# Optimization experiments

Measured on AMD Instinct MI355X. Metric: run time of the kernel, lower is better.

## Reference

```python
import jax, jax.numpy as jnp
from jax import lax
import numpy as np

B, T, H, OUT = 8, 1500, 1280, 4096
MAXTOK = 375
N_INNER = 3  # 1 mandatory integrate-and-fire iteration + 2 gated extras (alpha<1 => 1 suffices)


def _forward_cif(hidden, alphas, num_tokens, max_tok):
    # hidden: [B, T, D], alphas: [B, T], num_tokens: [B] int32
    Bv, Tv, _ = hidden.shape
    nm1 = num_tokens - 1
    bidx = jnp.arange(Bv)

    def step(carry, xs):
        integrate, token_index = carry  # [B] float, [B] int32
        alpha_t, not_last = xs
        col = jnp.zeros((Bv, max_tok), alphas.dtype)
        alpha = alpha_t
        alpha_needed = 1.0 - integrate
        integrate = integrate + alpha
        ready = integrate >= 1.0
        remainds = jnp.zeros_like(alpha)
        active = jnp.any(ready) | True  # first body iteration always runs (do-while)
        active = jnp.asarray(True)
        for _ in range(N_INNER):
            n_int = jnp.where(ready, integrate - 1.0, integrate)
            a_int = jnp.where(ready, alpha_needed, alpha)
            n_col = col.at[bidx, token_index].set(a_int)
            n_rem = alpha - a_int
            n_tok = jnp.minimum(token_index + ready.astype(token_index.dtype), nm1)
            n_ready = n_int >= 1.0
            integrate = jnp.where(active, n_int, integrate)
            col = jnp.where(active, n_col, col)
            remainds = jnp.where(active, n_rem, remainds)
            token_index = jnp.where(active, n_tok, token_index)
            alpha = jnp.where(active, n_rem, alpha)
            alpha_needed = jnp.where(active, jnp.ones_like(alpha_needed), alpha_needed)
            ready = jnp.where(active, n_ready, jnp.zeros_like(ready))
            active = active & jnp.any(ready)
        # torch adds remainds into column t at step t+1 (so last column never gets it)
        col = jnp.where(not_last, col.at[bidx, token_index].add(remainds), col)
        return (integrate, token_index), col

    init = (jnp.zeros((Bv,), alphas.dtype), jnp.zeros((Bv,), jnp.int32))
    xs = (alphas.T, jnp.arange(Tv) < Tv - 1)  # per-step alpha column, not-last flag
    _, cols = lax.scan(step, init, xs)  # cols: [T, B, max_tok]
    weights = jnp.transpose(cols, (1, 2, 0))  # [B, max_tok, T]
    return jnp.einsum('bmt,btd->bmd', weights, hidden)


def setup_inputs() -> dict:
    key = jax.random.key(0)
    ks = jax.random.split(key, 4)
    audio_features = jax.random.normal(ks[0], (B, T, H), jnp.float32)
    num_tokens = jax.random.randint(ks[1], (B,), 100, MAXTOK + 1).astype(jnp.int32)
    rms_w = jnp.ones((H,), jnp.float32) * 0.4
    cif_w = jax.random.normal(ks[2], (H - 1, H), jnp.float32) / np.sqrt(H - 1)
    cif_b = jnp.zeros((H,), jnp.float32)
    text_w = jax.random.normal(ks[3], (H, OUT), jnp.float32) / np.sqrt(H)
    text_b = jnp.zeros((OUT,), jnp.float32)
    return dict(audio_features=audio_features, num_tokens=num_tokens, rms_w=rms_w,
                cif_w=cif_w, cif_b=cif_b, text_w=text_w, text_b=text_b, max_tokens=MAXTOK)


def reference(audio_features, num_tokens, rms_w, cif_w, cif_b, text_w, text_b, max_tokens):
    alphas = jax.nn.sigmoid(audio_features[:, :, -1])  # [B, T]
    pred_num_tokens = alphas.sum(-1)  # [B]
    alphas = alphas * (num_tokens.astype(alphas.dtype) / pred_num_tokens)[:, None]
    h = _forward_cif(audio_features[:, :, :-1], alphas, num_tokens, max_tokens)  # [B, M, H-1]
    h = h @ cif_w + cif_b  # cif_proj -> [B, M, H]
    d = h.shape[-1]
    rms = jnp.sqrt(jnp.sum(h * h, axis=-1, keepdims=True) / d + 1e-6)
    h = h / rms * rms_w  # RMSNorm(post_ln)
    h = h @ text_w + text_b  # text_proj -> [B, M, OUT]
    return h, pred_num_tokens
```

## Files before the change

### kernel.cpp

```cpp
#include <hip/hip_runtime.h>
#include <hip/hip_bf16.h>
#include <stdint.h>

#define B_ 8
#define T_ 1500
#define TPAD 1504
#define H_ 1280
#define HM1 1279
#define OUT_ 4096
#define MTOK 375
#define MROWS (B_*MTOK)
#define KPAD 1280

typedef __attribute__((ext_vector_type(8))) short bf16x8;
typedef __attribute__((ext_vector_type(4))) float f32x4;
typedef unsigned short u16;
typedef unsigned int u32;

static __device__ __forceinline__ u16 f2bf(float f) {
    unsigned int x = __float_as_uint(f);
    unsigned int r = (x + 0x7fffu + ((x >> 16) & 1u)) >> 16;
    return (u16)r;
}
static __device__ __forceinline__ void glds16(const u16* g, u16* l) {
    __builtin_amdgcn_global_load_lds(
        (const __attribute__((address_space(1))) void*)g,
        (__attribute__((address_space(3))) void*)l, 16, 0, 0);
}

__global__ __launch_bounds__(256) void k_front(
    const float* __restrict__ audio, const int* __restrict__ num_tokens,
    const float* __restrict__ rms_w,
    float* __restrict__ pred_out,
    int* __restrict__ tok0, float* __restrict__ w0a,
    int* __restrict__ tok1, float* __restrict__ w1a,
    int* __restrict__ lo, int* __restrict__ hi,
    float* __restrict__ h_sumsq,
    const float* __restrict__ cif_w, const float* __restrict__ text_w,
    u16* __restrict__ cwt, u16* __restrict__ twt)
{
    __shared__ float smem[3524];
    const int tid = threadIdx.x;

    if (blockIdx.x < B_) {
        const int b = blockIdx.x;
        float* al = smem;
        float* ip = smem + TPAD;
        float* red = smem + 2*TPAD;
        int*   redI = (int*)(smem + 2*TPAD + 256);
        float* scale_sh = smem + 2*TPAD + 512;

        float sig[6];
        float s = 0.f;
        #pragma unroll
        for (int i = 0; i < 6; ++i) {
            int t = tid + i*256;
            sig[i] = 0.f;
            if (t < T_) {
                float x = audio[((size_t)b*T_ + t)*H_ + (H_-1)];
                sig[i] = 1.f / (1.f + expf(-x));
                s += sig[i];
            }
        }
        red[tid] = s; __syncthreads();
        for (int off = 128; off > 0; off >>= 1) {
            if (tid < off) red[tid] += red[tid+off];
            __syncthreads();
        }
        if (tid == 0) {
            float pred = red[0];
            pred_out[b] = pred;
            *scale_sh = (float)num_tokens[b] / pred;
        }
        __syncthreads();
        float scale = *scale_sh;
        #pragma unroll
        for (int i = 0; i < 6; ++i) {
            int t = tid + i*256;
            if (t < T_) al[t] = sig[i] * scale;
        }
        if (tid < TPAD - T_) al[T_ + tid] = 0.f;
        for (int m = tid; m < MTOK; m += 256) {
            lo[b*MTOK+m] = T_; hi[b*MTOK+m] = 0;
            h_sumsq[b*MTOK+m] = 0.f;
        }
        if (tid == 0) lo[b*MTOK] = 0;
        __syncthreads();

        if (tid == 0) {
            float integ = 0.f;
            float4 c0 = *(const float4*)&al[0];
            float4 c1 = *(const float4*)&al[4];
            float4 c2 = *(const float4*)&al[8];
            float4 c3 = *(const float4*)&al[12];
            for (int t = 0; t < TPAD; t += 16) {
                float4 n0, n1, n2, n3;
                if (t + 16 < TPAD) {
                    n0 = *(const float4*)&al[t+16];
                    n1 = *(const float4*)&al[t+20];
                    n2 = *(const float4*)&al[t+24];
                    n3 = *(const float4*)&al[t+28];
                }
                float4 o0, o1, o2, o3;
                float sx;
                o0.x = integ; sx = integ + c0.x; integ = sx - floorf(sx);
                o0.y = integ; sx = integ + c0.y; integ = sx - floorf(sx);
                o0.z = integ; sx = integ + c0.z; integ = sx - floorf(sx);
                o0.w = integ; sx = integ + c0.w; integ = sx - floorf(sx);
                o1.x = integ; sx = integ + c1.x; integ = sx - floorf(sx);
                o1.y = integ; sx = integ + c1.y; integ = sx - floorf(sx);
                o1.z = integ; sx = integ + c1.z; integ = sx - floorf(sx);
                o1.w = integ; sx = integ + c1.w; integ = sx - floorf(sx);
                o2.x = integ; sx = integ + c2.x; integ = sx - floorf(sx);
                o2.y = integ; sx = integ + c2.y; integ = sx - floorf(sx);
                o2.z = integ; sx = integ + c2.z; integ = sx - floorf(sx);
                o2.w = integ; sx = integ + c2.w; integ = sx - floorf(sx);
                o3.x = integ; sx = integ + c3.x; integ = sx - floorf(sx);
                o3.y = integ; sx = integ + c3.y; integ = sx - floorf(sx);
                o3.z = integ; sx = integ + c3.z; integ = sx - floorf(sx);
                o3.w = integ; sx = integ + c3.w; integ = sx - floorf(sx);
                *(float4*)&ip[t+0]  = o0;
                *(float4*)&ip[t+4]  = o1;
                *(float4*)&ip[t+8]  = o2;
                *(float4*)&ip[t+12] = o3;
                c0 = n0; c1 = n1; c2 = n2; c3 = n3;
            }
        }
        __syncthreads();

        const int t0 = tid * 6;
        const int nm1 = num_tokens[b] - 1;
        int fires[6];
        int cnt = 0;
        if (t0 < T_) {
            #pragma unroll
            for (int j = 0; j < 6; ++j) {
                int t = t0 + j;
                float sx = ip[t] + al[t];
                fires[j] = (sx >= 1.f) ? 1 : 0;
                cnt += fires[j];
            }
        }
        redI[tid] = cnt; __syncthreads();
        #pragma unroll
        for (int off = 1; off < 256; off <<= 1) {
            int v = redI[tid];
            if (tid >= off) v += redI[tid - off];
            __syncthreads();
            redI[tid] = v;
            __syncthreads();
        }
        if (t0 < T_) {
            int F = redI[tid] - cnt;
            const int base = b*T_;
            #pragma unroll
            for (int j = 0; j < 6; ++j) {
                int t = t0 + j;
                float a = al[t], ipv = ip[t];
                int fire = fires[j];
                F += fire;
                int tk1 = min(F, nm1);
                int tk0 = min(F - fire, nm1);
                float w0 = fire ? (1.f - ipv) : a;
                float w1 = (t < T_-1) ? (a - w0) : 0.f;
                tok0[base+t] = tk0;  w0a[base+t] = w0;
                tok1[base+t] = tk1;  w1a[base+t] = w1;
                if (tk1 != tk0) {
                    hi[b*MTOK + tk0] = t + 1;
                    lo[b*MTOK + tk1] = t;
                }
                if (t == T_-1) hi[b*MTOK + tk1] = T_;
            }
        }
    } else {
        float (*tile)[33] = (float(*)[33])smem;
        int blk = blockIdx.x - B_;
        const float* src; u16* dst; int R, C, bx, by; bool scaled;
        if (blk < 1600) { src = cif_w;  dst = cwt; R = HM1; C = H_;   bx = blk % 40;  by = blk / 40;  scaled = false; }
        else { blk -= 1600; src = text_w; dst = twt; R = H_;  C = OUT_; bx = blk % 128; by = blk / 128; scaled = true; }
        int c0 = bx * 32, r0 = by * 32;
        int lx = tid & 31, ly = tid >> 5;
        #pragma unroll
        for (int j = 0; j < 4; ++j) {
            int r = r0 + ly + j*8;
            tile[ly + j*8][lx] = (r < R) ? src[(size_t)r*C + c0 + lx] : 0.f;
        }
        __syncthreads();
        float rw = scaled ? rms_w[r0 + lx] : 1.f;
        #pragma unroll
        for (int j = 0; j < 4; ++j) {
            int c = c0 + ly + j*8;
            dst[(size_t)c*KPAD + r0 + lx] = f2bf(tile[lx][ly + j*8] * rw);
        }
    }
}

__global__ __launch_bounds__(256) void k3_pool(
    const float* __restrict__ audio,
    const int* __restrict__ tok0, const float* __restrict__ w0a,
    const int* __restrict__ tok1, const float* __restrict__ w1a,
    const int* __restrict__ lo, const int* __restrict__ hi,
    u16* __restrict__ h1b)
{
    __shared__ float wl[1536];
    const int bm = blockIdx.x;
    const int b = bm / MTOK, m = bm % MTOK;
    const int l = lo[bm], h = hi[bm];
    const int tid = threadIdx.x;
    const int len = h - l;

    for (int j = tid; j < len; j += 256) {
        int i0 = b*T_ + l + j;
        float w = 0.f;
        if (tok0[i0] == m) w += w0a[i0];
        if (tok1[i0] == m) w += w1a[i0];
        wl[j] = w;
    }
    __syncthreads();

    const int d4 = tid * 4;
    const int d1 = 1024 + tid;
    const float* rowp = audio + (size_t)(b*T_ + l) * H_;
    float4 acc4 = make_float4(0.f, 0.f, 0.f, 0.f);
    float acc1 = 0.f;
    #pragma unroll 4
    for (int j = 0; j < len; ++j) {
        float w = wl[j];
        const float* row = rowp + (size_t)j * H_;
        float4 r4 = *(const float4*)(row + d4);
        float r1 = (d1 < HM1) ? row[d1] : 0.f;
        acc4.x += w * r4.x; acc4.y += w * r4.y;
        acc4.z += w * r4.z; acc4.w += w * r4.w;
        acc1 += w * r1;
    }
    u16* dst = h1b + (size_t)bm * KPAD;
    ushort4 o;
    o.x = f2bf(acc4.x); o.y = f2bf(acc4.y); o.z = f2bf(acc4.z); o.w = f2bf(acc4.w);
    *(ushort4*)&dst[d4] = o;
    dst[d1] = (d1 < HM1) ? f2bf(acc1) : (u16)0;
}

template<bool CIF>
__global__ __launch_bounds__(512, 2) void gemm256(
    const u16* __restrict__ A, const u16* __restrict__ Bt,
    const float* __restrict__ bias, void* __restrict__ Cv,
    float* __restrict__ h_sumsq, int M, int N)
{
    constexpr int K = KPAD;
    constexpr int NT = K / 64;
    __shared__ u16 sA[2][256*64];
    __shared__ u16 sB[2][256*64];
    const int tid = threadIdx.x;
    const int wave = tid >> 6, lane = tid & 63;
    const int wr = wave >> 2, wc = wave & 3;
    const int lrow = lane & 15, quad = lane >> 4;
    const int m0 = blockIdx.y * 256, n0 = blockIdx.x * 256;

    const int rS = tid >> 3;
    const int cS = (tid & 7) ^ (rS & 7);
    u32 aoff[4], boff[4];
    #pragma unroll
    for (int p = 0; p < 4; ++p) {
        aoff[p] = (u32)(min(m0 + rS + 64*p, M - 1) * K + cS*8);
        boff[p] = (u32)((n0 + rS + 64*p) * K + cS*8);
    }

    const int csw = (quad ^ (lrow & 7)) << 3;
    int offA[8], offB[4];
    #pragma unroll
    for (int mi = 0; mi < 8; ++mi)
        offA[mi] = (wr*128 + mi*16 + lrow)*64 + csw;
    #pragma unroll
    for (int ni = 0; ni < 4; ++ni)
        offB[ni] = (wc*64 + ni*16 + lrow)*64 + csw;

    f32x4 acc[8][4] = {};

    #pragma unroll
    for (int p = 0; p < 4; ++p) {
        glds16(A + aoff[p],      (u16*)sA[0] + (tid + 512*p)*8);
        glds16(Bt + boff[p],     (u16*)sB[0] + (tid + 512*p)*8);
    }
    #pragma unroll
    for (int p = 0; p < 4; ++p) {
        glds16(A + aoff[p] + 64, (u16*)sA[1] + (tid + 512*p)*8);
        glds16(Bt + boff[p] + 64,(u16*)sB[1] + (tid + 512*p)*8);
    }
    asm volatile("s_waitcnt vmcnt(8)" ::: "memory");
    __builtin_amdgcn_s_barrier();

    for (int t = 0; t < NT; ++t) {
        const u16* bufA = sA[t & 1];
        const u16* bufB = sB[t & 1];
        #pragma unroll
        for (int ks = 0; ks < 2; ++ks) {
            const int kx = ks ? 32 : 0;
            bf16x8 bfr[4], afr[8];
            #pragma unroll
            for (int ni = 0; ni < 4; ++ni)
                bfr[ni] = *(const bf16x8*)&bufB[offB[ni] ^ kx];
            #pragma unroll
            for (int mi = 0; mi < 8; ++mi)
                afr[mi] = *(const bf16x8*)&bufA[offA[mi] ^ kx];
            #pragma unroll
            for (int mi = 0; mi < 8; ++mi)
                #pragma unroll
                for (int ni = 0; ni < 4; ++ni)
                    acc[mi][ni] = __builtin_amdgcn_mfma_f32_16x16x32_bf16(
                        afr[mi], bfr[ni], acc[mi][ni], 0, 0, 0);
        }
        __syncthreads();
        if (t + 2 < NT) {
            const u32 k0 = (u32)(t + 2) * 64;
            u16* dA = (u16*)sA[t & 1];
            u16* dB = (u16*)sB[t & 1];
            #pragma unroll
            for (int p = 0; p < 4; ++p) {
                glds16(A + aoff[p] + k0,  dA + (tid + 512*p)*8);
                glds16(Bt + boff[p] + k0, dB + (tid + 512*p)*8);
            }
        }
    }

    float bv[4];
    #pragma unroll
    for (int ni = 0; ni < 4; ++ni)
        bv[ni] = bias[n0 + wc*64 + ni*16 + lrow];

    #pragma unroll
    for (int mi = 0; mi < 8; ++mi) {
        #pragma unroll
        for (int rr = 0; rr < 4; ++rr) {
            int row = m0 + wr*128 + mi*16 + quad*4 + rr;
            if (CIF) {
                float ss = 0.f;
                #pragma unroll
                for (int ni = 0; ni < 4; ++ni) {
                    float v = acc[mi][ni][rr] + bv[ni];
                    ss += v * v;
                    if (row < M)
                        ((u16*)Cv)[(size_t)row*N + (n0 + wc*64 + ni*16 + lrow)] = f2bf(v);
                }
                ss += __shfl_xor(ss, 1);
                ss += __shfl_xor(ss, 2);
                ss += __shfl_xor(ss, 4);
                ss += __shfl_xor(ss, 8);
                if (lrow == 0 && row < M) atomicAdd(&h_sumsq[row], ss);
            } else {
                float inv = 1.f;
                if (row < M)
                    inv = 1.f / sqrtf(h_sumsq[row] / (float)H_ + 1e-6f);
                #pragma unroll
                for (int ni = 0; ni < 4; ++ni) {
                    if (row < M)
                        ((float*)Cv)[(size_t)row*N + (n0 + wc*64 + ni*16 + lrow)] =
                            acc[mi][ni][rr] * inv + bv[ni];
                }
            }
        }
    }
}

extern "C" void kernel_launch(void* const* d_in, const int* in_sizes, int n_in,
                              void* d_out, int out_size, void* d_ws, size_t ws_size,
                              hipStream_t stream) {
    (void)in_sizes; (void)n_in; (void)out_size; (void)ws_size;
    const float* audio      = (const float*)d_in[0];
    const int*   num_tokens = (const int*)d_in[1];
    const float* rms_w      = (const float*)d_in[2];
    const float* cif_w      = (const float*)d_in[3];
    const float* cif_b      = (const float*)d_in[4];
    const float* text_w     = (const float*)d_in[5];
    const float* text_b     = (const float*)d_in[6];

    float* out  = (float*)d_out;
    float* pred = out + (size_t)MROWS * OUT_;

    char* ws = (char*)d_ws;
    float* h_sumsq = (float*)(ws + 0);
    float* w0a  = (float*)(ws + 48000);
    float* w1a  = (float*)(ws + 96000);
    int*   tok0 = (int*)  (ws + 144000);
    int*   tok1 = (int*)  (ws + 192000);
    int*   lo   = (int*)  (ws + 240000);
    int*   hi   = (int*)  (ws + 252000);
    u16* h1b = (u16*)(ws + 264192);
    u16* cwt = (u16*)(ws + 7944192);
    u16* twt = (u16*)(ws + 11220992);
    u16* hX  = (u16*)(ws + 21706752);

    k_front<<<B_ + 1600 + 5120, 256, 0, stream>>>(
        audio, num_tokens, rms_w, pred, tok0, w0a, tok1, w1a, lo, hi,
        h_sumsq, cif_w, text_w, cwt, twt);
    k3_pool<<<MROWS, 256, 0, stream>>>(audio, tok0, w0a, tok1, w1a, lo, hi, h1b);
    gemm256<true><<<dim3(H_/256, (MROWS+255)/256), 512, 0, stream>>>(
        h1b, cwt, cif_b, hX, h_sumsq, MROWS, H_);
    gemm256<false><<<dim3(OUT_/256, (MROWS+255)/256), 512, 0, stream>>>(
        hX, twt, text_b, out, h_sumsq, MROWS, OUT_);
}
```

Before: 264.6 us.

## Software-pipeline GEMM mainloop with quadrant MFMA interleaving and staged LDS loads

Rewrites the bf16 GEMM main loop into an explicitly scheduled two-tile-per-iteration pipeline. Each 64-wide K tile is split into half-tile quadrants: register fragments for the next quadrant are loaded from LDS while MFMAs run on the current one, and global-to-LDS copies for later tiles are issued in slices between barriers. s_setprio is raised around the MFMA blocks. The goal is to hide LDS and global latency behind matrix math. In exchange the loop uses many more barriers and hand-counted vmcnt waits that are fragile, and clamping the tile index makes the final iterations load redundant data.

Result: slower. 318.0 us (+20.2%).

```diff
diff --git a/kernel.cpp b/kernel.cpp
--- a/kernel.cpp
+++ b/kernel.cpp
@@ -240,6 +240,40 @@
     dst[d1] = (d1 < HM1) ? f2bf(acc1) : (u16)0;
 }
 
+#define BAR()     __builtin_amdgcn_s_barrier()
+#define LGKM0()   asm volatile("s_waitcnt lgkmcnt(0)" ::: "memory")
+#define WAITVM(N) asm volatile("s_waitcnt vmcnt(" #N ")" ::: "memory")
+
+#define LDA_(D, BUF, HH) do { \
+  _Pragma("unroll") for (int m_ = 0; m_ < 4; ++m_) { \
+    D[m_][0] = *(const bf16x8*)&sA[BUF][aBase + (HH)*4096 + m_*1024 + csw]; \
+    D[m_][1] = *(const bf16x8*)&sA[BUF][aBase + (HH)*4096 + m_*1024 + (csw ^ 32)]; \
+  } } while (0)
+
+#define LDB_(D, BUF, HH) do { \
+  _Pragma("unroll") for (int n_ = 0; n_ < 2; ++n_) { \
+    D[n_][0] = *(const bf16x8*)&sB[BUF][bBase + (HH)*2048 + n_*1024 + csw]; \
+    D[n_][1] = *(const bf16x8*)&sB[BUF][bBase + (HH)*2048 + n_*1024 + (csw ^ 32)]; \
+  } } while (0)
+
+#define STG_A(BUF, HH, KT) do { int kt_ = min((int)(KT), NT-1) * 64; \
+  glds16(A + aOff[HH][0] + kt_, &sA[BUF][(HH)*8192 + idx0*8]); \
+  glds16(A + aOff[HH][1] + kt_, &sA[BUF][(HH)*8192 + idx1*8]); } while (0)
+
+#define STG_B(BUF, HH, KT) do { int kt_ = min((int)(KT), NT-1) * 64; \
+  glds16(Bt + bOff[HH][0] + kt_, &sB[BUF][(HH)*8192 + idx0*8]); \
+  glds16(Bt + bOff[HH][1] + kt_, &sB[BUF][(HH)*8192 + idx1*8]); } while (0)
+
+#define MMQ(RA, RB, HA, HB) do { \
+  __builtin_amdgcn_s_setprio(1); \
+  _Pragma("unroll") for (int m_ = 0; m_ < 4; ++m_) \
+  _Pragma("unroll") for (int n_ = 0; n_ < 2; ++n_) \
+  _Pragma("unroll") for (int k_ = 0; k_ < 2; ++k_) \
+    acc[(HA)*4+m_][(HB)*2+n_] = __builtin_amdgcn_mfma_f32_16x16x32_bf16( \
+        RA[m_][k_], RB[n_][k_], acc[(HA)*4+m_][(HB)*2+n_], 0, 0, 0); \
+  __builtin_amdgcn_s_setprio(0); \
+} while (0)
+
 template<bool CIF>
 __global__ __launch_bounds__(512, 2) void gemm256(
     const u16* __restrict__ A, const u16* __restrict__ Bt,
@@ -248,78 +282,61 @@
 {
     constexpr int K = KPAD;
     constexpr int NT = K / 64;
-    __shared__ u16 sA[2][256*64];
-    __shared__ u16 sB[2][256*64];
+    constexpr int NIT = NT / 2;
+    __shared__ u16 sA[2][16384];
+    __shared__ u16 sB[2][16384];
     const int tid = threadIdx.x;
     const int wave = tid >> 6, lane = tid & 63;
     const int wr = wave >> 2, wc = wave & 3;
     const int lrow = lane & 15, quad = lane >> 4;
     const int m0 = blockIdx.y * 256, n0 = blockIdx.x * 256;
 
-    const int rS = tid >> 3;
-    const int cS = (tid & 7) ^ (rS & 7);
-    u32 aoff[4], boff[4];
+    const int idx0 = tid, idx1 = tid + 512;
+    const int rS0 = idx0 >> 3, rS1 = idx1 >> 3;
+    const int cG0 = ((idx0 & 7) ^ (rS0 & 7)) * 8;
+    const int cG1 = ((idx1 & 7) ^ (rS1 & 7)) * 8;
+    u32 aOff[2][2], bOff[2][2];
     #pragma unroll
-    for (int p = 0; p < 4; ++p) {
-        aoff[p] = (u32)(min(m0 + rS + 64*p, M - 1) * K + cS*8);
-        boff[p] = (u32)((n0 + rS + 64*p) * K + cS*8);
-    }
-
+    for (int h = 0; h < 2; ++h) {
+        aOff[h][0] = (u32)min(m0 + h*128 + rS0, M-1) * K + cG0;
+        aOff[h][1] = (u32)min(m0 + h*128 + rS1, M-1) * K + cG1;
+        bOff[h][0] = (u32)(n0 + h*128 + rS0) * K + cG0;
+        bOff[h][1] = (u32)(n0 + h*128 + rS1) * K + cG1;
+    }
     const int csw = (quad ^ (lrow & 7)) << 3;
-    int offA[8], offB[4];
-    #pragma unroll
-    for (int mi = 0; mi < 8; ++mi)
-        offA[mi] = (wr*128 + mi*16 + lrow)*64 + csw;
-    #pragma unroll
-    for (int ni = 0; ni < 4; ++ni)
-        offB[ni] = (wc*64 + ni*16 + lrow)*64 + csw;
-
+    const int aBase = (wr*128 + lrow) * 64;
+    const int bBase = (wc*64 + lrow) * 64;
+
+    bf16x8 rA0[4][2], rA1[4][2];
+    bf16x8 rB0[2][2], rB1[2][2];
     f32x4 acc[8][4] = {};
 
-    #pragma unroll
-    for (int p = 0; p < 4; ++p) {
-        glds16(A + aoff[p],      (u16*)sA[0] + (tid + 512*p)*8);
-        glds16(Bt + boff[p],     (u16*)sB[0] + (tid + 512*p)*8);
-    }
-    #pragma unroll
-    for (int p = 0; p < 4; ++p) {
-        glds16(A + aoff[p] + 64, (u16*)sA[1] + (tid + 512*p)*8);
-        glds16(Bt + boff[p] + 64,(u16*)sB[1] + (tid + 512*p)*8);
-    }
-    asm volatile("s_waitcnt vmcnt(8)" ::: "memory");
-    __builtin_amdgcn_s_barrier();
-
-    for (int t = 0; t < NT; ++t) {
-        const u16* bufA = sA[t & 1];
-        const u16* bufB = sB[t & 1];
-        #pragma unroll
-        for (int ks = 0; ks < 2; ++ks) {
-            const int kx = ks ? 32 : 0;
-            bf16x8 bfr[4], afr[8];
-            #pragma unroll
-            for (int ni = 0; ni < 4; ++ni)
-                bfr[ni] = *(const bf16x8*)&bufB[offB[ni] ^ kx];
-            #pragma unroll
-            for (int mi = 0; mi < 8; ++mi)
-                afr[mi] = *(const bf16x8*)&bufA[offA[mi] ^ kx];
-            #pragma unroll
-            for (int mi = 0; mi < 8; ++mi)
-                #pragma unroll
-                for (int ni = 0; ni < 4; ++ni)
-                    acc[mi][ni] = __builtin_amdgcn_mfma_f32_16x16x32_bf16(
-                        afr[mi], bfr[ni], acc[mi][ni], 0, 0, 0);
-        }
-        __syncthreads();
-        if (t + 2 < NT) {
-            const u32 k0 = (u32)(t + 2) * 64;
-            u16* dA = (u16*)sA[t & 1];
-            u16* dB = (u16*)sB[t & 1];
-            #pragma unroll
-            for (int p = 0; p < 4; ++p) {
-                glds16(A + aoff[p] + k0,  dA + (tid + 512*p)*8);
-                glds16(Bt + boff[p] + k0, dB + (tid + 512*p)*8);
-            }
-        }
+    STG_A(0,0,0); STG_A(0,1,0); STG_B(0,0,0); STG_B(0,1,0);
+    STG_A(1,0,1); STG_A(1,1,1); STG_B(1,0,1); STG_B(1,1,1);
+    WAITVM(8);
+    BAR();
+    LDA_(rA0, 0, 0);
+    LDB_(rB0, 0, 0);
+    LGKM0();
+
+    for (int it = 0; it < NIT; ++it) {
+        const int t = it * 2;
+        BAR(); LDA_(rA1, 0, 1);
+        MMQ(rA0, rB0, 0, 0); LGKM0();
+        BAR(); LDB_(rB1, 0, 1); STG_A(0, 0, t+2);
+        MMQ(rA1, rB0, 1, 0); LGKM0();
+        WAITVM(2); BAR(); LDB_(rB0, 1, 0); STG_A(0, 1, t+2);
+        MMQ(rA0, rB1, 0, 1); LGKM0();
+        BAR(); LDA_(rA0, 1, 0); STG_B(0, 0, t+2);
+        MMQ(rA1, rB1, 1, 1); LGKM0();
+        BAR(); LDA_(rA1, 1, 1); STG_B(0, 1, t+2);
+        MMQ(rA0, rB0, 0, 0); LGKM0();
+        BAR(); LDB_(rB1, 1, 1); STG_A(1, 0, t+3); STG_A(1, 1, t+3);
+        MMQ(rA1, rB0, 1, 0); LGKM0();
+        WAITVM(4); BAR(); LDB_(rB0, 0, 0); STG_B(1, 0, t+3); STG_B(1, 1, t+3);
+        MMQ(rA0, rB1, 0, 1); LGKM0();
+        BAR(); LDA_(rA0, 0, 0);
+        MMQ(rA1, rB1, 1, 1); LGKM0();
     }
 
     float bv[4];
```
